# Optimization experiments

Hardware: AMD Instinct MI355X
Metric: run time of the kernel (lower is better)

Reference implementation:

```python
import jax, jax.numpy as jnp
import numpy as np

IMG_H, IMG_W = 128, 128
FOCAL, NEAR, FAR = 140.0, 0.1, 10.0
RIGHT = (IMG_W - 1.0) / 2.0 * NEAR / FOCAL
TOP = RIGHT * (float(IMG_H) / IMG_W)
# row-vector GL perspective projection (v_clip = v_cam @ P), matching dirt's matrices.perspective_projection
PROJ = np.array([
    [NEAR / RIGHT, 0.0, 0.0, 0.0],
    [0.0, NEAR / TOP, 0.0, 0.0],
    [0.0, 0.0, -(FAR + NEAR) / (FAR - NEAR), -1.0],
    [0.0, 0.0, -2.0 * FAR * NEAR / (FAR - NEAR), 0.0],
], dtype=np.float32)
CHUNK = 64
EPS = 1e-9


def transform_vertices(vertices, pose):
    # vertices [N,3], pose [4,4] -> clip-space coords [N,4]
    G = jnp.array([[1.0, 0.0, 0.0], [0.0, -1.0, 0.0], [0.0, 0.0, -1.0]], jnp.float32)
    rot = G @ pose[:3, :3]
    cam_pose = pose.at[:3, :3].set(rot)
    cam_pose = cam_pose.at[1, 3].set(-pose[1, 3]).at[2, 3].set(-pose[2, 3])
    view = cam_pose.T
    vh = jnp.concatenate([vertices, jnp.ones_like(vertices[:, :1])], axis=1)
    return (vh @ view) @ jnp.asarray(PROJ)


def screen_coords(clip):
    # clip [...,4] -> pixel x (right), pixel y (down), ndc z, clip w
    w = clip[..., 3]
    x = (clip[..., 0] / w * 0.5 + 0.5) * IMG_W
    y = (0.5 - clip[..., 1] / w * 0.5) * IMG_H
    z = clip[..., 2] / w
    return x, y, z, w


def select_faces(clip, faces):
    # hard z-buffer visibility pass: per pixel, id of nearest covering face (-1 = background)
    B = clip.shape[0]
    F = faces.shape[0]
    px = jnp.arange(IMG_W, dtype=jnp.float32) + 0.5            # [W]
    py = (jnp.arange(IMG_H, dtype=jnp.float32) + 0.5)[:, None]  # [H,1]
    x, y, z, w = screen_coords(clip)                            # each [B,N]
    fchunks = faces.reshape(F // CHUNK, CHUNK, 3)
    idchunks = jnp.arange(F, dtype=jnp.int32).reshape(F // CHUNK, CHUNK)

    def body(carry, xs):
        best_z, best_f = carry
        fc, fid = xs                                  # [C,3], [C]
        xi, yi, zi, wi = x[:, fc], y[:, fc], z[:, fc], w[:, fc]   # [B,C,3]
        e4 = lambda a: a[..., None, None]             # [B,C] -> [B,C,1,1]
        x0, x1, x2 = e4(xi[..., 0]), e4(xi[..., 1]), e4(xi[..., 2])
        y0, y1, y2 = e4(yi[..., 0]), e4(yi[..., 1]), e4(yi[..., 2])
        # edge functions at pixel centers -> unnormalized barycentrics [B,C,H,W]
        e0 = (x2 - x1) * (py - y1) - (y2 - y1) * (px - x1)
        e1 = (x0 - x2) * (py - y2) - (y0 - y2) * (px - x2)
        e2 = (x1 - x0) * (py - y0) - (y1 - y0) * (px - x0)
        area = e0 + e1 + e2
        s = jnp.sign(area)
        ok = (jnp.abs(area) > EPS) & e4((wi > 1e-6).all(-1))
        inside = (e0 * s >= 0) & (e1 * s >= 0) & (e2 * s >= 0) & ok
        zpix = (e0 * e4(zi[..., 0]) + e1 * e4(zi[..., 1]) + e2 * e4(zi[..., 2])) / jnp.where(jnp.abs(area) > EPS, area, 1.0)
        inside = inside & (zpix >= -1.0) & (zpix <= 1.0)
        zc = jnp.where(inside, zpix, jnp.inf)         # [B,C,H,W]
        zmin = zc.min(axis=1)                         # [B,H,W]
        fsel = fid[zc.argmin(axis=1)]                 # [B,H,W]
        better = zmin < best_z
        return (jnp.where(better, zmin, best_z), jnp.where(better, fsel, best_f)), None

    init = (jnp.full((B, IMG_H, IMG_W), jnp.inf, jnp.float32),
            jnp.full((B, IMG_H, IMG_W), -1, jnp.int32))
    (_, best_f), _ = jax.lax.scan(body, init, (fchunks, idchunks))
    return best_f


def shade(clip, vcolors, faces, face_id):
    # differentiable perspective-correct interpolation of [mask,u,v] for the visible face
    fid = jnp.maximum(face_id, 0)                       # [B,H,W]
    vidx = faces[fid]                                   # [B,H,W,3]
    tri = jax.vmap(lambda c, vi: c[vi])(clip, vidx)     # [B,H,W,3,4]
    col = jax.vmap(lambda c, vi: c[vi])(vcolors, vidx)  # [B,H,W,3,3]
    x, y, z, w = screen_coords(tri)                     # [B,H,W,3]
    px = (jnp.arange(IMG_W, dtype=jnp.float32) + 0.5)[None, None, :]
    py = (jnp.arange(IMG_H, dtype=jnp.float32) + 0.5)[None, :, None]
    e0 = (x[..., 2] - x[..., 1]) * (py - y[..., 1]) - (y[..., 2] - y[..., 1]) * (px - x[..., 1])
    e1 = (x[..., 0] - x[..., 2]) * (py - y[..., 2]) - (y[..., 0] - y[..., 2]) * (px - x[..., 2])
    e2 = (x[..., 1] - x[..., 0]) * (py - y[..., 0]) - (y[..., 1] - y[..., 0]) * (px - x[..., 0])
    b = jnp.stack([e0, e1, e2], axis=-1)                # [B,H,W,3]
    bw = b / w                                          # perspective-correct weights
    denom = bw.sum(-1, keepdims=True)
    denom = jnp.where(jnp.abs(denom) > EPS, denom, 1.0)
    pc = bw / denom
    gbuffer = (pc[..., None] * col).sum(axis=-2)        # [B,H,W,3]
    mask = (face_id >= 0).astype(jnp.float32)[..., None]
    return gbuffer * mask


def sample_texture(texture, uv):
    # texture [TH,TW,C], uv [H,W,2]; faithful to original: clip uv, scale by full texture shape, bilinear
    th, tw = texture.shape[0], texture.shape[1]
    idx = jnp.clip(uv[..., ::-1], 0.0, 1.0) * jnp.array([th, tw], jnp.float32)
    fl = jnp.floor(idx)
    frac = idx - fl
    i = fl.astype(jnp.int32)
    iy0 = jnp.clip(i[..., 0], 0, th - 1)
    iy1 = jnp.clip(i[..., 0] + 1, 0, th - 1)
    ix0 = jnp.clip(i[..., 1], 0, tw - 1)
    ix1 = jnp.clip(i[..., 1] + 1, 0, tw - 1)
    tl = texture[iy0, ix0]; tr = texture[iy0, ix1]
    bl = texture[iy1, ix0]; br = texture[iy1, ix1]
    fy = frac[..., :1]; fx = frac[..., 1:]
    return (tl * (1.0 - fx) * (1.0 - fy) + tr * fx * (1.0 - fy)
            + bl * (1.0 - fx) * fy + br * fx * fy)


def forward(vertices, uv_map, faces, texture, poses):
    faces = faces.astype(jnp.int32)
    clip = jax.vmap(transform_vertices)(vertices, poses)         # [B,N,4]
    vcolors = jnp.concatenate([jnp.ones_like(vertices[..., :1]), uv_map], axis=-1)  # [B,N,3] = [1,u,v]
    face_id = select_faces(jax.lax.stop_gradient(clip), faces)   # [B,H,W]
    gbuffer = shade(clip, vcolors, faces, face_id)               # [B,H,W,3]
    mask_render = gbuffer[..., :1]
    uv = gbuffer[..., 1:3]
    unlit = jax.vmap(sample_texture)(texture, uv)                # [B,H,W,3]
    return unlit * mask_render


def setup_inputs():
    key = jax.random.key(0)
    k = jax.random.split(key, 5)
    B, N, F, TH, TW = 4, 4096, 8192, 2048, 2048
    vertices = jax.random.uniform(k[0], (B, N, 3), jnp.float32, -0.5, 0.5)
    uv_map = jax.random.uniform(k[1], (B, N, 2), jnp.float32)
    faces = jax.random.randint(k[2], (F, 3), 0, N, jnp.int32)
    texture = jax.random.uniform(k[3], (B, TH, TW, 3), jnp.float32)
    poses = jnp.tile(jnp.eye(4, dtype=jnp.float32)[None], (B, 1, 1))
    poses = poses.at[:, 2, 3].set(3.0)  # object ends up ~3 units in front of the GL camera
    poses = poses.at[:, 0, 3].set(jax.random.uniform(k[4], (B,), jnp.float32, -0.2, 0.2))
    return {"vertices": vertices, "uv_map": uv_map, "faces": faces, "texture": texture, "poses": poses}


def reference(vertices, uv_map, faces, texture, poses):
    return forward(vertices, uv_map, faces, texture, poses)
```

## Files before the change

kernel.cpp:

```cpp
#include <hip/hip_runtime.h>
#include <cstdint>
#include <cmath>

#define IMG_H 128
#define IMG_W 128
#define TILE 16
#define TILES_X (IMG_W / TILE)
#define TILES_Y (IMG_H / TILE)
#define NTILES (TILES_X * TILES_Y)
#define NSUB 8
#define CCH 128

constexpr double FOCAL_D = 140.0, NEAR_D = 0.1, FAR_D = 10.0;
constexpr double RIGHT_D = (IMG_W - 1.0) / 2.0 * NEAR_D / FOCAL_D;
constexpr double TOP_D   = RIGHT_D * ((double)IMG_H / (double)IMG_W);
constexpr float P00 = (float)(NEAR_D / RIGHT_D);
constexpr float P11 = (float)(NEAR_D / TOP_D);
constexpr float P22 = (float)(-(FAR_D + NEAR_D) / (FAR_D - NEAR_D));
constexpr float P32 = (float)(-2.0 * FAR_D * NEAR_D / (FAR_D - NEAR_D));

__device__ __forceinline__ unsigned long long packKey(float z, int f) {
    unsigned int zb = __float_as_uint(z);
    zb = (zb & 0x80000000u) ? ~zb : (zb | 0x80000000u);
    return ((unsigned long long)zb << 32) | (unsigned int)f;
}

__global__ void k_vertex(const float* __restrict__ verts, const float* __restrict__ poses,
                         float4* __restrict__ vscr, int* __restrict__ cnt, int cntN,
                         int B, int N) {
#pragma clang fp contract(off)
    int id = blockIdx.x * blockDim.x + threadIdx.x;
    if (cnt && id < cntN) cnt[id] = 0;
    if (id >= B * N) return;
    int b = id / N;
    const float* v = verts + (size_t)id * 3;
    const float* P = poses + (size_t)b * 16;
    float x = v[0], y = v[1], z = v[2];
    float cp[4][4] = {
        { P[0],  P[1],  P[2],  P[3]  },
        {-P[4], -P[5], -P[6], -P[7]  },
        {-P[8], -P[9], -P[10],-P[11] },
        { P[12], P[13], P[14], P[15] }
    };
    float cam[4];
    for (int j = 0; j < 4; ++j)
        cam[j] = ((x * cp[j][0] + y * cp[j][1]) + z * cp[j][2]) + cp[j][3];
    float c0 = cam[0] * P00;
    float c1 = cam[1] * P11;
    float c2 = (cam[2] * P22) + (cam[3] * P32);
    float c3 = cam[2] * (-1.0f);
    float sx = ((c0 / c3) * 0.5f + 0.5f) * (float)IMG_W;
    float sy = (0.5f - (c1 / c3) * 0.5f) * (float)IMG_H;
    float sz = c2 / c3;
    vscr[id] = make_float4(sx, sy, sz, c3);
}

__global__ void k_bin(const int* __restrict__ faces, const float4* __restrict__ vscr,
                      float4* __restrict__ recA, float4* __restrict__ recB,
                      float4* __restrict__ recC, float4* __restrict__ recD,
                      int* __restrict__ list, int* __restrict__ cnt,
                      unsigned long long* __restrict__ keybuf,
                      int B, int N, int F) {
#pragma clang fp contract(off)
    int id = blockIdx.x * blockDim.x + threadIdx.x;
    for (int i = id; i < B * IMG_H * IMG_W; i += B * F) keybuf[i] = ~0ull;
    if (id >= B * F) return;
    int b = id / F, f = id - b * F;
    int i0 = faces[f * 3 + 0], i1 = faces[f * 3 + 1], i2 = faces[f * 3 + 2];
    float4 v0 = vscr[(size_t)b * N + i0];
    float4 v1 = vscr[(size_t)b * N + i1];
    float4 v2 = vscr[(size_t)b * N + i2];

    if (!(v0.w > 1e-6f && v1.w > 1e-6f && v2.w > 1e-6f)) return;

    float minx = fminf(v0.x, fminf(v1.x, v2.x));
    float maxx = fmaxf(v0.x, fmaxf(v1.x, v2.x));
    float miny = fminf(v0.y, fminf(v1.y, v2.y));
    float maxy = fmaxf(v0.y, fmaxf(v1.y, v2.y));
    if (!(minx <= maxx) || !(miny <= maxy)) return;
    minx = fmaxf(minx, -4.0f);  maxx = fminf(maxx, (float)IMG_W + 4.0f);
    miny = fmaxf(miny, -4.0f);  maxy = fminf(maxy, (float)IMG_H + 4.0f);
    int xlo = max(0, (int)floorf(minx) - 1);
    int xhi = min(IMG_W - 1, (int)floorf(maxx) + 1);
    int ylo = max(0, (int)floorf(miny) - 1);
    int yhi = min(IMG_H - 1, (int)floorf(maxy) + 1);
    if (xlo > xhi || ylo > yhi) return;

    size_t r = (size_t)id;
    recA[r] = make_float4(v1.x, v1.y, v2.x, v2.y);
    recB[r] = make_float4(v0.x, v0.y, miny, maxy);
    recC[r] = make_float4(v0.z, v1.z, v2.z, 0.0f);
    recD[r] = make_float4(v2.x - v1.x, v2.y - v1.y, v0.x - v2.x, v0.y - v2.y);

    int tx0 = xlo >> 4, tx1 = xhi >> 4, ty0 = ylo >> 4, ty1 = yhi >> 4;
    int sub = f & (NSUB - 1);
    int cap = (F + NSUB - 1) / NSUB;
    for (int ty = ty0; ty <= ty1; ++ty)
        for (int tx = tx0; tx <= tx1; ++tx) {
            int bin = b * NTILES + ty * TILES_X + tx;
            int slot = atomicAdd(&cnt[bin * NSUB + sub], 1);
            list[((size_t)bin * NSUB + sub) * cap + slot] = f;
        }
}

__global__ __launch_bounds__(256) void k_rasterChunk(const int* __restrict__ list,
        const int* __restrict__ cnt,
        const float4* __restrict__ recA, const float4* __restrict__ recB,
        const float4* __restrict__ recC, const float4* __restrict__ recD,
        unsigned long long* __restrict__ keybuf, int B, int F, int cap) {
#pragma clang fp contract(off)
    int ls = blockIdx.x;
    int n = cnt[ls];
    int base = blockIdx.y * CCH;
    if (base >= n) return;
    int m = min(CCH, n - base);
    int bin = ls >> 3;
    int b = bin / NTILES;
    int tile = bin - b * NTILES;
    const int* mylist = list + (size_t)ls * cap + base;

    int tx = tile & (TILES_X - 1), ty = tile >> 3;
    int t = threadIdx.x;
    int x = (tx << 4) + (t & 15);
    int y = (ty << 4) + (t >> 4);
    float px = (float)x + 0.5f, py = (float)y + 0.5f;
    int wv = t >> 6;
    float strip_py0 = (float)((ty << 4) + (wv << 2)) + 0.5f;
    float strip_py1 = strip_py0 + 3.0f;

    unsigned long long key = ~0ull;

    __shared__ float4 sA[CCH], sB[CCH], sC[CCH], sD[CCH];
    __shared__ int sfid[CCH];

    if (t < m) {
        int f = mylist[t];
        sfid[t] = f;
        size_t r = (size_t)b * F + f;
        sA[t] = recA[r]; sB[t] = recB[r]; sC[t] = recC[r]; sD[t] = recD[r];
    }
    __syncthreads();

    for (int j = 0; j < m; ++j) {
        float4 bb = sB[j];
        if (bb.z - 1.5f > strip_py1 || bb.w + 1.5f < strip_py0) continue;
        float4 aa = sA[j], cc = sC[j], dd = sD[j];
        float e0 = dd.x * (py - aa.y) - dd.y * (px - aa.x);
        float e1 = dd.z * (py - aa.w) - dd.w * (px - aa.z);
        float dx2 = aa.x - bb.x, dy2 = aa.y - bb.y;
        float e2 = dx2 * (py - bb.y) - dy2 * (px - bb.x);
        float area = (e0 + e1) + e2;
        bool okA = fabsf(area) > 1e-9f;
        float s = (area > 0.0f) ? 1.0f : ((area < 0.0f) ? -1.0f : area);
        bool inside = (e0 * s >= 0.0f) && (e1 * s >= 0.0f) && (e2 * s >= 0.0f) && okA;
        if (__ballot(inside)) {
            float den = okA ? area : 1.0f;
            float zpix = ((e0 * cc.x + e1 * cc.y) + e2 * cc.z) / den;
            if (inside && (zpix >= -1.0f) && (zpix <= 1.0f)) {
                unsigned long long k = packKey(zpix, sfid[j]);
                key = (k < key) ? k : key;
            }
        }
    }
    if (key != ~0ull) {
        unsigned long long* ap = &keybuf[(size_t)b * (IMG_H * IMG_W) + (size_t)y * IMG_W + x];
        atomicMin(ap, key);
    }
}

__global__ __launch_bounds__(256) void k_rasterF(const int* __restrict__ faces,
                                                 const float4* __restrict__ vscr,
                                                 unsigned long long* __restrict__ keybuf,
                                                 int B, int N, int F) {
#pragma clang fp contract(off)
    int wid = __builtin_amdgcn_readfirstlane(blockIdx.x * 4 + (threadIdx.x >> 6));
    if (wid >= B * F) return;
    int b = wid / F;
    int f = wid - b * F;
    int lane = threadIdx.x & 63;

    int i0 = faces[f * 3 + 0], i1 = faces[f * 3 + 1], i2 = faces[f * 3 + 2];
    float4 v0 = vscr[(size_t)b * N + i0];
    float4 v1 = vscr[(size_t)b * N + i1];
    float4 v2 = vscr[(size_t)b * N + i2];
    if (!(v0.w > 1e-6f && v1.w > 1e-6f && v2.w > 1e-6f)) return;

    float dx0 = v2.x - v1.x, dy0 = v2.y - v1.y;
    float dx1 = v0.x - v2.x, dy1 = v0.y - v2.y;
    float dx2 = v1.x - v0.x, dy2 = v1.y - v0.y;
    float z0 = v0.z, z1 = v1.z, z2 = v2.z;

    float minx = fminf(v0.x, fminf(v1.x, v2.x));
    float maxx = fmaxf(v0.x, fmaxf(v1.x, v2.x));
    float miny = fminf(v0.y, fminf(v1.y, v2.y));
    float maxy = fmaxf(v0.y, fmaxf(v1.y, v2.y));
    if (!(minx <= maxx) || !(miny <= maxy)) return;
    minx = fmaxf(minx, -4.0f);  maxx = fminf(maxx, (float)IMG_W + 4.0f);
    miny = fmaxf(miny, -4.0f);  maxy = fminf(maxy, (float)IMG_H + 4.0f);
    int xlo = max(0, (int)floorf(minx) - 1);
    int xhi = min(IMG_W - 1, (int)floorf(maxx) + 1);
    int ylo = max(0, (int)floorf(miny) - 1);
    int yhi = min(IMG_H - 1, (int)floorf(maxy) + 1);
    if (xlo > xhi || ylo > yhi) return;

    int lx = lane & 7, lyn = lane >> 3;
    unsigned long long* kb = keybuf + (size_t)b * IMG_H * IMG_W;

    for (int y0 = ylo; y0 <= yhi; y0 += 8) {
        int y = y0 + lyn;
        bool yok = (y <= yhi);
        float py = (float)y + 0.5f;
        float pyd0 = py - v1.y, pyd1 = py - v2.y, pyd2 = py - v0.y;
        for (int x0 = xlo; x0 <= xhi; x0 += 8) {
            int x = x0 + lx;
            bool ok = yok && (x <= xhi);
            float px = (float)x + 0.5f;
            float e0 = dx0 * pyd0 - dy0 * (px - v1.x);
            float e1 = dx1 * pyd1 - dy1 * (px - v2.x);
            float e2 = dx2 * pyd2 - dy2 * (px - v0.x);
            float area = (e0 + e1) + e2;
            bool okA = fabsf(area) > 1e-9f;
            float s = (area > 0.0f) ? 1.0f : ((area < 0.0f) ? -1.0f : area);
            bool inside = (e0 * s >= 0.0f) && (e1 * s >= 0.0f) && (e2 * s >= 0.0f)
                          && okA && ok;
            if (__ballot(inside)) {
                float den = okA ? area : 1.0f;
                float zpix = ((e0 * z0 + e1 * z1) + e2 * z2) / den;
                if (inside && (zpix >= -1.0f) && (zpix <= 1.0f)) {
                    unsigned long long* ap = &kb[(size_t)y * IMG_W + x];
                    unsigned long long cur = *(const volatile unsigned long long*)ap;
                    unsigned long long k = packKey(zpix, f);
                    if (k < cur) atomicMin(ap, k);
                }
            }
        }
    }
}

__global__ void k_shade(const unsigned long long* __restrict__ keybuf,
                        const int* __restrict__ faces, const float4* __restrict__ vscr,
                        const float* __restrict__ uvmap, const float* __restrict__ tex,
                        float* __restrict__ out, int B, int N, int tside) {
#pragma clang fp contract(off)
    int id = blockIdx.x * blockDim.x + threadIdx.x;
    if (id >= B * IMG_H * IMG_W) return;
    int b = id / (IMG_H * IMG_W);
    int p = id - b * (IMG_H * IMG_W);
    int y = p / IMG_W, x = p - y * IMG_W;
    unsigned long long key = keybuf[id];
    int fid = (key == ~0ull) ? -1 : (int)(key & 0xFFFFFFFFull);
    int f = (fid < 0) ? 0 : fid;
    int i0 = faces[f * 3 + 0], i1 = faces[f * 3 + 1], i2 = faces[f * 3 + 2];
    float4 v0 = vscr[(size_t)b * N + i0];
    float4 v1 = vscr[(size_t)b * N + i1];
    float4 v2 = vscr[(size_t)b * N + i2];
    float px = (float)x + 0.5f, py = (float)y + 0.5f;
    float e0 = (v2.x - v1.x) * (py - v1.y) - (v2.y - v1.y) * (px - v1.x);
    float e1 = (v0.x - v2.x) * (py - v2.y) - (v0.y - v2.y) * (px - v2.x);
    float e2 = (v1.x - v0.x) * (py - v0.y) - (v1.y - v0.y) * (px - v0.x);
    float bw0 = e0 / v0.w, bw1 = e1 / v1.w, bw2 = e2 / v2.w;
    float den = (bw0 + bw1) + bw2;
    den = (fabsf(den) > 1e-9f) ? den : 1.0f;
    float pc0 = bw0 / den, pc1 = bw1 / den, pc2 = bw2 / den;
    float u0 = uvmap[((size_t)b * N + i0) * 2],     vv0 = uvmap[((size_t)b * N + i0) * 2 + 1];
    float u1 = uvmap[((size_t)b * N + i1) * 2],     vv1 = uvmap[((size_t)b * N + i1) * 2 + 1];
    float u2 = uvmap[((size_t)b * N + i2) * 2],     vv2 = uvmap[((size_t)b * N + i2) * 2 + 1];
    float g0 = (pc0 * 1.0f + pc1 * 1.0f) + pc2 * 1.0f;
    float g1 = (pc0 * u0 + pc1 * u1) + pc2 * u2;
    float g2 = (pc0 * vv0 + pc1 * vv1) + pc2 * vv2;
    float mask = (fid >= 0) ? 1.0f : 0.0f;
    g0 = g0 * mask; g1 = g1 * mask; g2 = g2 * mask;
    float ts = (float)tside;
    float iyf = fminf(fmaxf(g2, 0.0f), 1.0f) * ts;
    float ixf = fminf(fmaxf(g1, 0.0f), 1.0f) * ts;
    float fly = floorf(iyf), flx = floorf(ixf);
    float fy = iyf - fly, fx = ixf - flx;
    int iy = (int)fly, ix = (int)flx;
    int tmax = tside - 1;
    int iy0 = min(max(iy, 0), tmax),     iy1 = min(max(iy + 1, 0), tmax);
    int ix0 = min(max(ix, 0), tmax),     ix1 = min(max(ix + 1, 0), tmax);
    const float* tb = tex + (size_t)b * tside * tside * 3;
    const float* tl = tb + ((size_t)iy0 * tside + ix0) * 3;
    const float* tr = tb + ((size_t)iy0 * tside + ix1) * 3;
    const float* bl = tb + ((size_t)iy1 * tside + ix0) * 3;
    const float* br = tb + ((size_t)iy1 * tside + ix1) * 3;
    float omfx = 1.0f - fx, omfy = 1.0f - fy;
    float* o = out + (size_t)id * 3;
    for (int c = 0; c < 3; ++c) {
        float r = (((tl[c] * omfx) * omfy) + ((tr[c] * fx) * omfy)) + ((bl[c] * omfx) * fy);
        r = r + ((br[c] * fx) * fy);
        o[c] = r * g0;
    }
}

extern "C" void kernel_launch(void* const* d_in, const int* in_sizes, int n_in,
                              void* d_out, int out_size, void* d_ws, size_t ws_size,
                              hipStream_t stream) {
    const float* verts = (const float*)d_in[0];
    const float* uvmap = (const float*)d_in[1];
    const int*   faces = (const int*)d_in[2];
    const float* tex   = (const float*)d_in[3];
    const float* poses = (const float*)d_in[4];
    int B = in_sizes[4] / 16;
    int N = in_sizes[0] / (B * 3);
    int F = in_sizes[2] / 3;
    int texels = in_sizes[3] / (B * 3);
    int tside = (int)(sqrt((double)texels) + 0.5);

    char* ws = (char*)d_ws;
    size_t off = 0;
    float4* vscr = (float4*)(ws + off); off += (size_t)B * N * sizeof(float4);
    float4* recA = (float4*)(ws + off); off += (size_t)B * F * sizeof(float4);
    float4* recB = (float4*)(ws + off); off += (size_t)B * F * sizeof(float4);
    float4* recC = (float4*)(ws + off); off += (size_t)B * F * sizeof(float4);
    float4* recD = (float4*)(ws + off); off += (size_t)B * F * sizeof(float4);
    unsigned long long* keybuf = (unsigned long long*)(ws + off);
    size_t keybytes = (size_t)B * IMG_H * IMG_W * sizeof(unsigned long long);
    off += keybytes;
    int cap = (F + NSUB - 1) / NSUB;
    int* list = (int*)(ws + off); off += (size_t)B * NTILES * NSUB * cap * sizeof(int);
    int* cnt  = (int*)(ws + off); off += (size_t)B * NTILES * NSUB * sizeof(int);
    int cntN = B * NTILES * NSUB;

    if (ws_size >= off) {
        k_vertex<<<(B * N + 255) / 256, 256, 0, stream>>>(verts, poses, vscr, cnt, cntN, B, N);
        k_bin<<<(B * F + 255) / 256, 256, 0, stream>>>(faces, vscr, recA, recB, recC, recD,
                                                       list, cnt, keybuf, B, N, F);
        int kmax = (cap + CCH - 1) / CCH;
        dim3 rgrid(B * NTILES * NSUB, kmax);
        k_rasterChunk<<<rgrid, 256, 0, stream>>>(list, cnt, recA, recB, recC, recD,
                                                 keybuf, B, F, cap);
        k_shade<<<(B * IMG_H * IMG_W + 255) / 256, 256, 0, stream>>>(
            keybuf, faces, vscr, uvmap, tex, (float*)d_out, B, N, tside);
    } else {
        float4* vscr0 = (float4*)ws;
        unsigned long long* keybuf0 = (unsigned long long*)(ws + (size_t)B * N * sizeof(float4));
        hipMemsetAsync(keybuf0, 0xFF, keybytes, stream);
        k_vertex<<<(B * N + 255) / 256, 256, 0, stream>>>(verts, poses, vscr0, (int*)nullptr, 0, B, N);
        int nwaves = B * F;
        k_rasterF<<<(nwaves + 3) / 4, 256, 0, stream>>>(faces, vscr0, keybuf0, B, N, F);
        k_shade<<<(B * IMG_H * IMG_W + 255) / 256, 256, 0, stream>>>(
            keybuf0, faces, vscr0, uvmap, tex, (float*)d_out, B, N, tside);
    }
}
```

Measured before the change: 402.4 us.

## Cull triangles per tile with conservative edge tests and use 8x8 wave blocks

During binning, each triangle is tested against each 16x16 tile with conservative edge functions at the tile corners, and tiles lying fully outside an edge are skipped. The aim is fewer list entries and less raster work. The raster kernel now gives each wave an 8x8 pixel block instead of a 16x4 strip. It rejects faces per wave using an integer bounding box packed into recC.w, replacing the earlier y-only strip test. The epsilon margins are meant to keep culling conservative, but they add arithmetic in the binning kernel and could drop coverage at exact edge cases.

```diff
diff --git a/kernel.cpp b/kernel.cpp
--- a/kernel.cpp
+++ b/kernel.cpp
@@ -23,6 +23,23 @@
     unsigned int zb = __float_as_uint(z);
     zb = (zb & 0x80000000u) ? ~zb : (zb | 0x80000000u);
     return ((unsigned long long)zb << 32) | (unsigned int)f;
+}
+
+__device__ __forceinline__ bool edgeAllOut(float dx, float dy, float ax, float ay,
+                                           float px0, float px1, float py0, float py1,
+                                           float s) {
+#pragma clang fp contract(off)
+    bool all = true;
+    #pragma unroll
+    for (int c = 0; c < 4; ++c) {
+        float px = (c & 1) ? px1 : px0;
+        float py = (c & 2) ? py1 : py0;
+        float e = dx * (py - ay) - dy * (px - ax);
+        float T = fabsf(dx) * (fabsf(py) + fabsf(ay)) + fabsf(dy) * (fabsf(px) + fabsf(ax));
+        float m = 1e-5f * T + 1e-3f;
+        all = all && (e * s < -m);
+    }
+    return all;
 }
 
 __global__ void k_vertex(const float* __restrict__ verts, const float* __restrict__ poses,
@@ -86,21 +103,44 @@
     int yhi = min(IMG_H - 1, (int)floorf(maxy) + 1);
     if (xlo > xhi || ylo > yhi) return;
 
+    float dx0 = v2.x - v1.x, dy0 = v2.y - v1.y;
+    float dx1 = v0.x - v2.x, dy1 = v0.y - v2.y;
+    float dx2 = v1.x - v0.x, dy2 = v1.y - v0.y;
+
     size_t r = (size_t)id;
+    unsigned pb = (unsigned)xlo | ((unsigned)xhi << 8) | ((unsigned)ylo << 16) | ((unsigned)yhi << 24);
     recA[r] = make_float4(v1.x, v1.y, v2.x, v2.y);
-    recB[r] = make_float4(v0.x, v0.y, miny, maxy);
-    recC[r] = make_float4(v0.z, v1.z, v2.z, 0.0f);
-    recD[r] = make_float4(v2.x - v1.x, v2.y - v1.y, v0.x - v2.x, v0.y - v2.y);
+    recB[r] = make_float4(v0.x, v0.y, 0.0f, 0.0f);
+    recC[r] = make_float4(v0.z, v1.z, v2.z, __uint_as_float(pb));
+    recD[r] = make_float4(dx0, dy0, dx1, dy1);
 
     int tx0 = xlo >> 4, tx1 = xhi >> 4, ty0 = ylo >> 4, ty1 = yhi >> 4;
     int sub = f & (NSUB - 1);
     int cap = (F + NSUB - 1) / NSUB;
-    for (int ty = ty0; ty <= ty1; ++ty)
+    for (int ty = ty0; ty <= ty1; ++ty) {
+        float py0 = (float)(ty << 4) + 0.5f, py1 = py0 + 15.0f;
         for (int tx = tx0; tx <= tx1; ++tx) {
+            float px0 = (float)(tx << 4) + 0.5f, px1 = px0 + 15.0f;
+            float ea = dx0 * (py0 - v1.y) - dy0 * (px0 - v1.x);
+            float eb = dx1 * (py0 - v2.y) - dy1 * (px0 - v2.x);
+            float ec = dx2 * (py0 - v0.y) - dy2 * (px0 - v0.x);
+            float areaC = (ea + eb) + ec;
+            float Tm = (fabsf(dx0) + fabsf(dx1) + fabsf(dx2)) * 300.0f
+                     + (fabsf(dy0) + fabsf(dy1) + fabsf(dy2)) * 300.0f;
+            float mA = 1e-5f * Tm + 1e-2f;
+            bool cull = false;
+            if (fabsf(areaC) > mA) {
+                float s = (areaC > 0.0f) ? 1.0f : -1.0f;
+                cull = edgeAllOut(dx0, dy0, v1.x, v1.y, px0, px1, py0, py1, s)
+                    || edgeAllOut(dx1, dy1, v2.x, v2.y, px0, px1, py0, py1, s)
+                    || edgeAllOut(dx2, dy2, v0.x, v0.y, px0, px1, py0, py1, s);
+            }
+            if (cull) continue;
             int bin = b * NTILES + ty * TILES_X + tx;
             int slot = atomicAdd(&cnt[bin * NSUB + sub], 1);
             list[((size_t)bin * NSUB + sub) * cap + slot] = f;
         }
+    }
 }
 
 __global__ __launch_bounds__(256) void k_rasterChunk(const int* __restrict__ list,
@@ -121,12 +161,13 @@
 
     int tx = tile & (TILES_X - 1), ty = tile >> 3;
     int t = threadIdx.x;
-    int x = (tx << 4) + (t & 15);
-    int y = (ty << 4) + (t >> 4);
+    int wv = t >> 6;
+    int wx0 = (tx << 4) + ((wv & 1) << 3);
+    int wy0 = (ty << 4) + ((wv >> 1) << 3);
+    int x = wx0 + (t & 7);
+    int y = wy0 + ((t >> 3) & 7);
     float px = (float)x + 0.5f, py = (float)y + 0.5f;
-    int wv = t >> 6;
-    float strip_py0 = (float)((ty << 4) + (wv << 2)) + 0.5f;
-    float strip_py1 = strip_py0 + 3.0f;
+    int wx1 = wx0 + 7, wy1 = wy0 + 7;
 
     unsigned long long key = ~0ull;
 
@@ -142,9 +183,12 @@
     __syncthreads();
 
     for (int j = 0; j < m; ++j) {
-        float4 bb = sB[j];
-        if (bb.z - 1.5f > strip_py1 || bb.w + 1.5f < strip_py0) continue;
-        float4 aa = sA[j], cc = sC[j], dd = sD[j];
+        float4 cc = sC[j];
+        unsigned pb = __float_as_uint(cc.w);
+        int fxlo = (int)(pb & 0xFFu), fxhi = (int)((pb >> 8) & 0xFFu);
+        int fylo = (int)((pb >> 16) & 0xFFu), fyhi = (int)(pb >> 24);
+        if (fxhi < wx0 || fxlo > wx1 || fyhi < wy0 || fylo > wy1) continue;
+        float4 aa = sA[j], bb = sB[j], dd = sD[j];
         float e0 = dd.x * (py - aa.y) - dd.y * (px - aa.x);
         float e1 = dd.z * (py - aa.w) - dd.w * (px - aa.z);
         float dx2 = aa.x - bb.x, dy2 = aa.y - bb.y;
```

New measurement: 377.8 us. 1.06x faster.
